# Performance work log

Hardware: AMD Instinct MI355X
Metric: run time of the kernel (lower is better)

The kernel has to match this reference:

```python
import jax, jax.numpy as jnp
import numpy as np

B, L, D, DI = 4, 4096, 2048, 256
LN_EPS = 1e-5


def setup_inputs() -> dict:
    key = jax.random.key(0)
    ks = jax.random.split(key, 5)
    x = jax.random.normal(ks[0], (B, L, D), jnp.float32)
    # xavier-ish scale for in/out projections, std=0.01 for scan projections (as in _init_weights)
    W_in = jax.random.normal(ks[1], (D, DI), jnp.float32) * np.float32(1.0 / np.sqrt(D))
    W_fwd = jax.random.normal(ks[2], (DI, 2 * DI), jnp.float32) * np.float32(0.01)
    W_bwd = jax.random.normal(ks[3], (DI, 2 * DI), jnp.float32) * np.float32(0.01)
    W_out = jax.random.normal(ks[4], (2 * DI, D), jnp.float32) * np.float32(1.0 / np.sqrt(2 * DI))
    gamma = jnp.ones((D,), jnp.float32)
    beta = jnp.zeros((D,), jnp.float32)
    return {"x": x, "W_in": W_in, "W_fwd": W_fwd, "W_bwd": W_bwd, "W_out": W_out, "gamma": gamma, "beta": beta}


def _scan_dir(z, Wp):
    """Gated linear recurrence h_t = delta_t * h_{t-1} + gate_t, with delta/gate from one GEMM.
    z: [B, L, d]; Wp: [d, 2d] -> returns [B, L, d]."""
    d = z.shape[-1]
    o = jnp.einsum("bld,de->ble", z, Wp)          # [B, L, 2d]
    delta = jax.nn.sigmoid(o[..., :d])             # [B, L, d]
    gate = o[..., d:] * z                          # [B, L, d]

    def step(h, dg):
        dlt, g = dg
        h = h * dlt + g
        return h, h

    h0 = jnp.zeros_like(z[:, 0])                   # [B, d]
    _, hs = jax.lax.scan(step, h0, (jnp.swapaxes(delta, 0, 1), jnp.swapaxes(gate, 0, 1)))
    return jnp.swapaxes(hs, 0, 1)                  # [B, L, d]


def reference(x, W_in, W_fwd, W_bwd, W_out, gamma, beta):
    z = jnp.einsum("bld,de->ble", x, W_in)         # [B, L, DI]
    h_fwd = _scan_dir(z, W_fwd)
    h_bwd = _scan_dir(z[:, ::-1], W_bwd)[:, ::-1]
    out = jnp.einsum("ble,ed->bld", jnp.concatenate([h_fwd, h_bwd], axis=-1), W_out)
    y = out + x                                    # residual
    mu = jnp.mean(y, axis=-1, keepdims=True)
    var = jnp.var(y, axis=-1, keepdims=True)
    return (y - mu) * jax.lax.rsqrt(var + LN_EPS) * gamma + beta
```

## Files before the change

kernel.cpp:

```cpp
#include <hip/hip_runtime.h>
#include <hip/hip_bf16.h>

using bf16 = __hip_bfloat16;
typedef float float4v __attribute__((ext_vector_type(4)));
typedef __bf16 bf16x8 __attribute__((ext_vector_type(8)));
typedef unsigned short ushort4v __attribute__((ext_vector_type(4)));
typedef unsigned short ushort8v __attribute__((ext_vector_type(8)));

#define B_  4
#define L_  4096
#define D_  2048
#define DI_ 256
#define M_  (B_*L_)
#define NC  64
#define LC  (L_/NC)

__device__ inline float bf2f(bf16 x) { return __bfloat162float(x); }
__device__ inline bf16  f2bf(float x) { return __float2bfloat16(x); }

__device__ inline void store4bf(bf16* p, float4v v) {
    ushort4v u;
#pragma unroll
    for (int i = 0; i < 4; i++) {
        bf16 h = f2bf(v[i]);
        u[i] = *(unsigned short*)&h;
    }
    *(ushort4v*)p = u;
}

__device__ inline float4v load4bf(const bf16* p) {
    ushort4v u = *(const ushort4v*)p;
    float4v v;
#pragma unroll
    for (int i = 0; i < 4; i++) v[i] = __uint_as_float(((unsigned)u[i]) << 16);
    return v;
}

__device__ inline ushort8v cvt8(float4v a, float4v b) {
    ushort8v u;
#pragma unroll
    for (int i = 0; i < 4; i++) {
        bf16 h0 = f2bf(a[i]); u[i]     = *(unsigned short*)&h0;
        bf16 h1 = f2bf(b[i]); u[i + 4] = *(unsigned short*)&h1;
    }
    return u;
}

__device__ __forceinline__ void gload_lds16(const bf16* g, bf16* l) {
    __builtin_amdgcn_global_load_lds((const __attribute__((address_space(1))) void*)(g),
                                     (__attribute__((address_space(3))) void*)(l),
                                     16, 0, 0);
}

template<int N> __device__ __forceinline__ void vmwait() {
    asm volatile("s_waitcnt vmcnt(%0)" :: "n"(N) : "memory");
}
template<int N> __device__ __forceinline__ void vmwait_lgkm0() {
    asm volatile("s_waitcnt vmcnt(%0) lgkmcnt(0)" :: "n"(N) : "memory");
}
__device__ __forceinline__ void bar() {
    asm volatile("" ::: "memory");
    __builtin_amdgcn_s_barrier();
    asm volatile("" ::: "memory");
}

__global__ void transpose_cvt(const float* __restrict__ in, bf16* __restrict__ out,
                              int R, int C, int obase) {
    int idx = blockIdx.x * 256 + threadIdx.x;
    if (idx < R * C) {
        int r = idx / C, c = idx - r * C;
        out[(size_t)(c + obase) * R + r] = f2bf(in[idx]);
    }
}


template<int TBM, int TBN, int BKT, int EPI, bool AF32>
__global__ __launch_bounds__(256) void gemm_bt(const void* __restrict__ Av,
                                               const bf16* __restrict__ BT,
                                               int K, int N,
                                               bf16* __restrict__ o0, bf16* __restrict__ o1,
                                               bf16* __restrict__ o2, bf16* __restrict__ o3,
                                               const bf16* __restrict__ auxb,
                                               const float* __restrict__ auxf) {
    constexpr int MI  = TBM / 32, NI = TBN / 32;
    constexpr int SLOTS = BKT / 8;
    constexpr int RPI   = 64 / SLOTS;
    constexpr int API   = TBM * SLOTS / 256;
    constexpr int BPI   = TBN * SLOTS / 256;
    constexpr int AP  = TBM / 64;
    constexpr int AI  = 2 * AP;
    constexpr int ASZ = TBM * BKT, BSZ = TBN * BKT;
    constexpr int ND  = AF32 ? 3 : 2;
    __shared__ __align__(16) bf16 As[ND * ASZ];
    __shared__ __align__(16) bf16 Bs[ND * BSZ];
    const int tid  = threadIdx.x;
    const int bm   = blockIdx.x, bn = blockIdx.y;
    const int lane = tid & 63, wave = tid >> 6;
    const int wm   = (wave >> 1) * (TBM / 2), wn = (wave & 1) * (TBN / 2);
    const int l15  = lane & 15, quad = lane >> 4;
    const int srow  = lane / SLOTS;
    const int sslot = lane % SLOTS;
    const int kslot = sslot ^ ((BKT == 32) ? ((srow >> 1) & 3) : (srow & 7));
    const int sr    = tid >> 2, scs = tid & 3;
    const int swslot = scs ^ ((sr >> 1) & 3);

    float4v acc[MI][NI] = {};
    const float* Af = (const float*)Av;
    const bf16*  Ab = (const bf16*)Av;
    float4v fa0[AP][2], fa1[AP][2], fa2[AP][2];

    const int nt   = K / BKT;
    const int mask = nt - 1;
    const int t0   = AF32 ? ((bm * 5 + bn * 3) & mask) : 0;
    auto T = [&](int i) { return ((i + t0) & mask) * BKT; };

    auto stage_a = [&](int buf, int kk) {
#pragma unroll
        for (int p = 0; p < API; p++) {
            int rbase = wave * (TBM / 4) + p * RPI;
            gload_lds16(Ab + (size_t)(bm * TBM + rbase + srow) * K + kk + kslot * 8,
                        As + buf * ASZ + rbase * BKT + lane * 8);
        }
    };
    auto stage_b = [&](int buf, int kk) {
#pragma unroll
        for (int p = 0; p < BPI; p++) {
            int rbase = wave * (TBN / 4) + p * RPI;
            gload_lds16(BT + (size_t)(bn * TBN + rbase + srow) * K + kk + kslot * 8,
                        Bs + buf * BSZ + rbase * BKT + lane * 8);
        }
    };
    auto load_a_f32 = [&](float4v (&fa)[AP][2], int kk) {
#pragma unroll
        for (int p = 0; p < AP; p++) {
            const float* src = Af + (size_t)(bm * TBM + p * 64 + sr) * K + kk + scs * 8;
            fa[p][0] = *(const float4v*)src;
            fa[p][1] = *(const float4v*)(src + 4);
        }
    };
    auto write_a_f32 = [&](float4v (&fa)[AP][2], int buf) {
#pragma unroll
        for (int p = 0; p < AP; p++)
            *(ushort8v*)(As + buf * ASZ + (p * 64 + sr) * BKT + swslot * 8)
                = cvt8(fa[p][0], fa[p][1]);
    };
    auto compute = [&](int buf) {
#pragma unroll
        for (int h = 0; h < BKT / 32; h++) {
            const int s = (BKT == 32) ? (quad ^ ((l15 >> 1) & 3))
                                      : ((quad + 4 * h) ^ (l15 & 7));
            bf16x8 af[MI], bfr[NI];
#pragma unroll
            for (int mi = 0; mi < MI; mi++)
                af[mi] = *(const bf16x8*)(As + buf * ASZ + (wm + mi * 16 + l15) * BKT + s * 8);
#pragma unroll
            for (int ni = 0; ni < NI; ni++)
                bfr[ni] = *(const bf16x8*)(Bs + buf * BSZ + (wn + ni * 16 + l15) * BKT + s * 8);
            __builtin_amdgcn_s_setprio(1);
#pragma unroll
            for (int mi = 0; mi < MI; mi++)
#pragma unroll
                for (int ni = 0; ni < NI; ni++)
                    acc[mi][ni] = __builtin_amdgcn_mfma_f32_16x16x32_bf16(
                        bfr[ni], af[mi], acc[mi][ni], 0, 0, 0);
            __builtin_amdgcn_s_setprio(0);
        }
    };

    if constexpr (AF32) {
        load_a_f32(fa0, T(0)); stage_b(0, T(0));
        load_a_f32(fa1, T(1)); stage_b(1, T(1));
        load_a_f32(fa2, T(2)); stage_b(2, T(2));
        vmwait<2 * AI + 3 * BPI>();
        write_a_f32(fa0, 0);

        auto body = [&](int t, int bi, int nbuf,
                        float4v (&fcur)[AP][2], float4v (&fnext)[AP][2]) {
            int k = nt - 1 - t;
            if (k >= 2)      vmwait_lgkm0<2 * (AI + BPI)>();
            else if (k == 1) vmwait_lgkm0<AI + BPI>();
            else             vmwait_lgkm0<0>();
            bar();
            compute(bi);
            bar();
            if (t + 3 < nt) { load_a_f32(fcur, T(t + 3)); stage_b(bi, T(t + 3)); }
            if (t + 1 < nt) {
                if (t + 3 < nt)      vmwait<2 * AI + 3 * BPI>();
                else if (t + 2 < nt) vmwait<AI + 2 * BPI>();
                else                 vmwait<BPI>();
                write_a_f32(fnext, nbuf);
            }
        };
        int t = 0;
        for (; t + 3 <= nt; t += 3) {
            body(t,     0, 1, fa0, fa1);
            body(t + 1, 1, 2, fa1, fa2);
            body(t + 2, 2, 0, fa2, fa0);
        }
        if (t < nt)     body(t,     0, 1, fa0, fa1);
        if (t + 1 < nt) body(t + 1, 1, 2, fa1, fa2);
    } else {
        stage_a(0, 0);     stage_b(0, 0);
        stage_a(1, BKT);   stage_b(1, BKT);
        for (int t = 0; t < nt; t++) {
            if (t == nt - 1) vmwait<0>(); else vmwait<API + BPI>();
            bar();
            compute(t & 1);
            bar();
            if (t + 2 < nt) {
                stage_a(t & 1, (t + 2) * BKT);
                stage_b(t & 1, (t + 2) * BKT);
            }
        }
    }

#pragma unroll
    for (int mi = 0; mi < MI; mi++) {
#pragma unroll
        for (int ni = 0; ni < NI; ni++) {
            int row = bm * TBM + wm + mi * 16 + l15;
            int col = bn * TBN + wn + ni * 16 + quad * 4;
            float4v v = acc[mi][ni];
            if (EPI == 0) {
                store4bf(o0 + (size_t)row * N + col, v);
            } else if (EPI == 1) {
                int sel = col >> 8, d = col & 255;
                bf16* dst = (sel == 0) ? o0 : (sel == 1) ? o1 : (sel == 2) ? o2 : o3;
                if (sel & 1) {
                    float4v z4 = load4bf(auxb + (size_t)row * DI_ + d);
#pragma unroll
                    for (int i = 0; i < 4; i++) v[i] *= z4[i];
                } else {
#pragma unroll
                    for (int i = 0; i < 4; i++) v[i] = 1.f / (1.f + __expf(-v[i]));
                }
                store4bf(dst + (size_t)row * DI_ + d, v);
            } else {
                float4v r = *(const float4v*)(auxf + (size_t)row * N + col);
#pragma unroll
                for (int i = 0; i < 4; i++) v[i] += r[i];
                store4bf(o0 + (size_t)row * N + col, v);
            }
        }
    }
}

__global__ __launch_bounds__(256) void scan_agg(const bf16* __restrict__ del_f,
                                                const bf16* __restrict__ gat_f,
                                                const bf16* __restrict__ del_b,
                                                const bf16* __restrict__ gat_b,
                                                float* __restrict__ aggA,
                                                float* __restrict__ aggB) {
    int c = blockIdx.x, b = blockIdx.y, dir = blockIdx.z, d = threadIdx.x;
    const bf16* delta = dir ? del_b : del_f;
    const bf16* gate  = dir ? gat_b : gat_f;
    float Ap = 1.f, h = 0.f;
    for (int i = 0; i < LC; i++) {
        int t = dir ? (L_ - 1 - (c * LC + i)) : (c * LC + i);
        size_t base = ((size_t)(b * L_ + t)) * DI_ + d;
        float dlt = bf2f(delta[base]);
        float g   = bf2f(gate[base]);
        Ap *= dlt;
        h = h * dlt + g;
    }
    size_t idx = (((size_t)dir * B_ + b) * NC + c) * DI_ + d;
    aggA[idx] = Ap;
    aggB[idx] = h;
}

__global__ void scan_mid(const float* __restrict__ aggA, const float* __restrict__ aggB,
                         float* __restrict__ Hin) {
    int b = blockIdx.x, dir = blockIdx.y, d = threadIdx.x;
    float h = 0.f;
    for (int c = 0; c < NC; c++) {
        size_t idx = (((size_t)dir * B_ + b) * NC + c) * DI_ + d;
        Hin[idx] = h;
        h = aggA[idx] * h + aggB[idx];
    }
}

__global__ __launch_bounds__(256) void scan_fix(const bf16* __restrict__ del_f,
                                                const bf16* __restrict__ gat_f,
                                                const bf16* __restrict__ del_b,
                                                const bf16* __restrict__ gat_b,
                                                const float* __restrict__ Hin,
                                                bf16* __restrict__ hcat) {
    int c = blockIdx.x, b = blockIdx.y, dir = blockIdx.z, d = threadIdx.x;
    const bf16* delta = dir ? del_b : del_f;
    const bf16* gate  = dir ? gat_b : gat_f;
    float h = Hin[(((size_t)dir * B_ + b) * NC + c) * DI_ + d];
    int colbase = dir * DI_;
    for (int i = 0; i < LC; i++) {
        int t = dir ? (L_ - 1 - (c * LC + i)) : (c * LC + i);
        size_t base = ((size_t)(b * L_ + t)) * DI_ + d;
        float dlt = bf2f(delta[base]);
        float g   = bf2f(gate[base]);
        h = h * dlt + g;
        hcat[((size_t)(b * L_ + t)) * (2 * DI_) + colbase + d] = f2bf(h);
    }
}

__global__ __launch_bounds__(256) void ln_kernel(const bf16* __restrict__ y,
                                                 const float* __restrict__ gamma,
                                                 const float* __restrict__ beta,
                                                 float* __restrict__ outp) {
    __shared__ float ss[4], ssq[4];
    int row = blockIdx.x, tid = threadIdx.x;
    size_t base = (size_t)row * D_ + tid * 8;
    uint4 raw = *(const uint4*)(y + base);
    const unsigned short* u = (const unsigned short*)&raw;
    float v[8];
    float s = 0.f, sq = 0.f;
#pragma unroll
    for (int i = 0; i < 8; i++) {
        v[i] = __uint_as_float(((unsigned)u[i]) << 16);
        s += v[i];
        sq += v[i] * v[i];
    }
    for (int o = 32; o > 0; o >>= 1) { s += __shfl_down(s, o); sq += __shfl_down(sq, o); }
    if ((tid & 63) == 0) { ss[tid >> 6] = s; ssq[tid >> 6] = sq; }
    __syncthreads();
    float S  = ss[0] + ss[1] + ss[2] + ss[3];
    float SQ = ssq[0] + ssq[1] + ssq[2] + ssq[3];
    float mean = S * (1.f / D_);
    float var  = SQ * (1.f / D_) - mean * mean;
    float rstd = rsqrtf(var + 1e-5f);
    float4v g0 = *(const float4v*)(gamma + tid * 8);
    float4v g1 = *(const float4v*)(gamma + tid * 8 + 4);
    float4v b0 = *(const float4v*)(beta + tid * 8);
    float4v b1 = *(const float4v*)(beta + tid * 8 + 4);
    float4v r0, r1;
#pragma unroll
    for (int i = 0; i < 4; i++) {
        r0[i] = (v[i] - mean) * rstd * g0[i] + b0[i];
        r1[i] = (v[i + 4] - mean) * rstd * g1[i] + b1[i];
    }
    *(float4v*)(outp + base)     = r0;
    *(float4v*)(outp + base + 4) = r1;
}

extern "C" void kernel_launch(void* const* d_in, const int* in_sizes, int n_in,
                              void* d_out, int out_size, void* d_ws, size_t ws_size,
                              hipStream_t stream) {
    (void)in_sizes; (void)n_in; (void)out_size; (void)ws_size;
    const float* x     = (const float*)d_in[0];
    const float* W_in  = (const float*)d_in[1];
    const float* W_fwd = (const float*)d_in[2];
    const float* W_bwd = (const float*)d_in[3];
    const float* W_out = (const float*)d_in[4];
    const float* gamma = (const float*)d_in[5];
    const float* beta  = (const float*)d_in[6];
    float* out = (float*)d_out;

    char* ws = (char*)d_ws;
    size_t off = 0;
    auto alloc = [&](size_t bytes) -> char* {
        char* p = ws + off;
        off += (bytes + 255) & ~(size_t)255;
        return p;
    };
    bf16*  WinT   = (bf16*)alloc((size_t)DI_ * D_ * 2);
    bf16*  WpT    = (bf16*)alloc((size_t)1024 * DI_ * 2);
    bf16*  WoutT  = (bf16*)alloc((size_t)D_ * 2 * DI_ * 2);
    bf16*  z      = (bf16*)alloc((size_t)M_ * DI_ * 2);
    bf16*  del_f  = (bf16*)alloc((size_t)M_ * DI_ * 2);
    bf16*  gat_f  = (bf16*)alloc((size_t)M_ * DI_ * 2);
    bf16*  del_b  = (bf16*)alloc((size_t)M_ * DI_ * 2);
    bf16*  gat_b  = (bf16*)alloc((size_t)M_ * DI_ * 2);
    bf16*  hcat   = (bf16*)alloc((size_t)M_ * 2 * DI_ * 2);
    bf16*  ybuf   = (bf16*)alloc((size_t)M_ * D_ * 2);
    float* aggA   = (float*)alloc((size_t)2 * B_ * NC * DI_ * 4);
    float* aggB   = (float*)alloc((size_t)2 * B_ * NC * DI_ * 4);
    float* Hin    = (float*)alloc((size_t)2 * B_ * NC * DI_ * 4);

    transpose_cvt<<<(D_ * DI_ + 255) / 256, 256, 0, stream>>>(W_in, WinT, D_, DI_, 0);
    transpose_cvt<<<(DI_ * 2 * DI_ + 255) / 256, 256, 0, stream>>>(W_fwd, WpT, DI_, 2 * DI_, 0);
    transpose_cvt<<<(DI_ * 2 * DI_ + 255) / 256, 256, 0, stream>>>(W_bwd, WpT, DI_, 2 * DI_, 2 * DI_);
    transpose_cvt<<<(2 * DI_ * D_ + 255) / 256, 256, 0, stream>>>(W_out, WoutT, 2 * DI_, D_, 0);

    gemm_bt<64, 128, 32, 0, true><<<dim3(M_ / 64, 2), 256, 0, stream>>>(
        x, WinT, D_, DI_, z, nullptr, nullptr, nullptr, nullptr, nullptr);

    gemm_bt<128, 128, 64, 1, false><<<dim3(M_ / 128, 1024 / 128), 256, 0, stream>>>(
        z, WpT, DI_, 1024, del_f, gat_f, del_b, gat_b, z, nullptr);

    scan_agg<<<dim3(NC, B_, 2), DI_, 0, stream>>>(del_f, gat_f, del_b, gat_b, aggA, aggB);
    scan_mid<<<dim3(B_, 2), DI_, 0, stream>>>(aggA, aggB, Hin);
    scan_fix<<<dim3(NC, B_, 2), DI_, 0, stream>>>(del_f, gat_f, del_b, gat_b, Hin, hcat);

    gemm_bt<128, 128, 64, 2, false><<<dim3(M_ / 128, D_ / 128), 256, 0, stream>>>(
        hcat, WoutT, 2 * DI_, D_, ybuf, nullptr, nullptr, nullptr, nullptr, x);

    ln_kernel<<<M_, 256, 0, stream>>>(ybuf, gamma, beta, out);
}
```

Measured before the change: 420.4 us.

## Triple-buffer bf16 GEMM mainloop, fuse weight transposes, shrink K-tile

Fuses the four weight transpose/convert launches into a single kernel. The bf16-input GEMM path moves from double to triple buffering: the next-next tile's global-to-LDS loads are issued inside the compute step, one barrier is dropped, and MFMA sections run at raised priority. The bf16 GEMMs also switch from BKT 64 to 32. This is meant to overlap loads with MFMA and cut launch and barrier overhead, at the cost of more LDS per block and more K iterations.

Result: no change. 415.2 us (-1.3%).

```diff
diff --git a/kernel.cpp b/kernel.cpp
--- a/kernel.cpp
+++ b/kernel.cpp
@@ -64,12 +64,33 @@
     asm volatile("" ::: "memory");
 }
 
-__global__ void transpose_cvt(const float* __restrict__ in, bf16* __restrict__ out,
-                              int R, int C, int obase) {
+__global__ __launch_bounds__(256) void transpose_all(const float* __restrict__ W_in,
+                                                     const float* __restrict__ W_fwd,
+                                                     const float* __restrict__ W_bwd,
+                                                     const float* __restrict__ W_out,
+                                                     bf16* __restrict__ WinT,
+                                                     bf16* __restrict__ WpT,
+                                                     bf16* __restrict__ WoutT) {
+    constexpr int S0 = D_ * DI_;
+    constexpr int S1 = DI_ * 2 * DI_;
+    constexpr int S2 = S1;
+    constexpr int S3 = 2 * DI_ * D_;
     int idx = blockIdx.x * 256 + threadIdx.x;
-    if (idx < R * C) {
-        int r = idx / C, c = idx - r * C;
-        out[(size_t)(c + obase) * R + r] = f2bf(in[idx]);
+    if (idx < S0) {
+        int r = idx / DI_, c = idx - r * DI_;
+        WinT[(size_t)c * D_ + r] = f2bf(W_in[idx]);
+    } else if (idx < S0 + S1) {
+        int j = idx - S0;
+        int r = j / (2 * DI_), c = j - r * (2 * DI_);
+        WpT[(size_t)c * DI_ + r] = f2bf(W_fwd[j]);
+    } else if (idx < S0 + S1 + S2) {
+        int j = idx - S0 - S1;
+        int r = j / (2 * DI_), c = j - r * (2 * DI_);
+        WpT[(size_t)(c + 2 * DI_) * DI_ + r] = f2bf(W_bwd[j]);
+    } else if (idx < S0 + S1 + S2 + S3) {
+        int j = idx - S0 - S1 - S2;
+        int r = j / D_, c = j - r * D_;
+        WoutT[(size_t)c * (2 * DI_) + r] = f2bf(W_out[j]);
     }
 }
 
@@ -90,9 +111,8 @@
     constexpr int AP  = TBM / 64;
     constexpr int AI  = 2 * AP;
     constexpr int ASZ = TBM * BKT, BSZ = TBN * BKT;
-    constexpr int ND  = AF32 ? 3 : 2;
-    __shared__ __align__(16) bf16 As[ND * ASZ];
-    __shared__ __align__(16) bf16 Bs[ND * BSZ];
+    __shared__ __align__(16) bf16 As[3 * ASZ];
+    __shared__ __align__(16) bf16 Bs[3 * BSZ];
     const int tid  = threadIdx.x;
     const int bm   = blockIdx.x, bn = blockIdx.y;
     const int lane = tid & 63, wave = tid >> 6;
@@ -202,16 +222,40 @@
     } else {
         stage_a(0, 0);     stage_b(0, 0);
         stage_a(1, BKT);   stage_b(1, BKT);
-        for (int t = 0; t < nt; t++) {
+        auto body3 = [&](int t, int bi, int nb) {
             if (t == nt - 1) vmwait<0>(); else vmwait<API + BPI>();
             bar();
-            compute(t & 1);
-            bar();
-            if (t + 2 < nt) {
-                stage_a(t & 1, (t + 2) * BKT);
-                stage_b(t & 1, (t + 2) * BKT);
+#pragma unroll
+            for (int h = 0; h < BKT / 32; h++) {
+                const int s = (BKT == 32) ? (quad ^ ((l15 >> 1) & 3))
+                                          : ((quad + 4 * h) ^ (l15 & 7));
+                bf16x8 af[MI], bfr[NI];
+#pragma unroll
+                for (int mi = 0; mi < MI; mi++)
+                    af[mi] = *(const bf16x8*)(As + bi * ASZ + (wm + mi * 16 + l15) * BKT + s * 8);
+                if (h == 0 && t + 2 < nt) stage_a(nb, (t + 2) * BKT);
+#pragma unroll
+                for (int ni = 0; ni < NI; ni++)
+                    bfr[ni] = *(const bf16x8*)(Bs + bi * BSZ + (wn + ni * 16 + l15) * BKT + s * 8);
+                if (h == 0 && t + 2 < nt) stage_b(nb, (t + 2) * BKT);
+                __builtin_amdgcn_s_setprio(1);
+#pragma unroll
+                for (int mi = 0; mi < MI; mi++)
+#pragma unroll
+                    for (int ni = 0; ni < NI; ni++)
+                        acc[mi][ni] = __builtin_amdgcn_mfma_f32_16x16x32_bf16(
+                            bfr[ni], af[mi], acc[mi][ni], 0, 0, 0);
+                __builtin_amdgcn_s_setprio(0);
             }
-        }
+        };
+        int t = 0;
+        for (; t + 3 <= nt; t += 3) {
+            body3(t,     0, 2);
+            body3(t + 1, 1, 0);
+            body3(t + 2, 2, 1);
+        }
+        if (t < nt)     body3(t,     0, 2);
+        if (t + 1 < nt) body3(t + 1, 1, 0);
     }
 
 #pragma unroll
@@ -373,22 +417,21 @@
     float* aggB   = (float*)alloc((size_t)2 * B_ * NC * DI_ * 4);
     float* Hin    = (float*)alloc((size_t)2 * B_ * NC * DI_ * 4);
 
-    transpose_cvt<<<(D_ * DI_ + 255) / 256, 256, 0, stream>>>(W_in, WinT, D_, DI_, 0);
-    transpose_cvt<<<(DI_ * 2 * DI_ + 255) / 256, 256, 0, stream>>>(W_fwd, WpT, DI_, 2 * DI_, 0);
-    transpose_cvt<<<(DI_ * 2 * DI_ + 255) / 256, 256, 0, stream>>>(W_bwd, WpT, DI_, 2 * DI_, 2 * DI_);
-    transpose_cvt<<<(2 * DI_ * D_ + 255) / 256, 256, 0, stream>>>(W_out, WoutT, 2 * DI_, D_, 0);
+    constexpr int TTOT = D_ * DI_ + 2 * DI_ * 2 * DI_ + 2 * DI_ * D_;
+    transpose_all<<<(TTOT + 255) / 256, 256, 0, stream>>>(
+        W_in, W_fwd, W_bwd, W_out, WinT, WpT, WoutT);
 
     gemm_bt<64, 128, 32, 0, true><<<dim3(M_ / 64, 2), 256, 0, stream>>>(
         x, WinT, D_, DI_, z, nullptr, nullptr, nullptr, nullptr, nullptr);
 
-    gemm_bt<128, 128, 64, 1, false><<<dim3(M_ / 128, 1024 / 128), 256, 0, stream>>>(
+    gemm_bt<128, 128, 32, 1, false><<<dim3(M_ / 128, 1024 / 128), 256, 0, stream>>>(
         z, WpT, DI_, 1024, del_f, gat_f, del_b, gat_b, z, nullptr);
 
     scan_agg<<<dim3(NC, B_, 2), DI_, 0, stream>>>(del_f, gat_f, del_b, gat_b, aggA, aggB);
     scan_mid<<<dim3(B_, 2), DI_, 0, stream>>>(aggA, aggB, Hin);
     scan_fix<<<dim3(NC, B_, 2), DI_, 0, stream>>>(del_f, gat_f, del_b, gat_b, Hin, hcat);
 
-    gemm_bt<128, 128, 64, 2, false><<<dim3(M_ / 128, D_ / 128), 256, 0, stream>>>(
+    gemm_bt<128, 128, 32, 2, false><<<dim3(M_ / 128, D_ / 128), 256, 0, stream>>>(
         hcat, WoutT, 2 * DI_, D_, ybuf, nullptr, nullptr, nullptr, nullptr, x);
 
     ln_kernel<<<M_, 256, 0, stream>>>(ybuf, gamma, beta, out);
```
